# Kernel optimization log

Hardware: AMD Instinct MI355X
Metric: run time of the kernel (lower is better)

The kernel has to match this reference:

```python
import jax, jax.numpy as jnp
import numpy as np

# Complete binary Huffman tree: V leaves, V-1 internal nodes, heap-indexed
# (node 0 = root, leaf i lives at heap index V-1+i, parent(n) = (n-1)//2).
V = 32768     # vocab size (leaves)
D = 15        # path depth = log2(V) internal nodes per leaf
DM = 1024     # input word-vector dim
B = 8         # batch of input word vectors
T = 1024      # target ids per batch item


def _build_paths():
    """paths[i, l] = heap index of the l-th internal node (leaf-to-root) on leaf i's path."""
    n = np.arange(V, dtype=np.int64) + (V - 1)  # leaf heap indices
    paths = np.zeros((V, D), dtype=np.int32)
    for lvl in range(D):
        n = (n - 1) // 2
        paths[:, lvl] = n
    return jnp.asarray(paths)


def setup_inputs() -> dict:
    key = jax.random.key(0)
    k1, k2, k3 = jax.random.split(key, 3)
    x = jax.random.normal(k1, (B, DM), dtype=jnp.float32)
    ids = jax.random.randint(k2, (B, T), 0, V)
    W = jax.random.normal(k3, (V - 1, DM), dtype=jnp.float32) * 0.02  # stacked Linear(DM,1) weights
    b = jnp.zeros((V - 1,), dtype=jnp.float32)                        # stacked Linear biases
    return {"x": x, "ids": ids, "paths": _build_paths(), "W": W, "b": b}


def reference(x, ids, paths, W, b):
    # node_idx: [B, T, D] internal-node heap indices along each target's path
    node_idx = paths[ids]
    Wp = W[node_idx]                 # [B, T, D, DM] gathered per-node weight rows
    bp = b[node_idx]                 # [B, T, D]
    # per-node Linear + bias: logit = w_node . x + b_node
    logits = jnp.einsum('btdk,bk->btd', Wp, x) + bp
    # product of sigmoid branch probabilities along the path -> [B, T]
    return jnp.prod(jax.nn.sigmoid(logits), axis=-1)
```

## Files before the change

kernel.cpp:

```cpp
#include <hip/hip_runtime.h>
#include <math.h>

#define V 32768
#define D 15
#define DM 1024
#define B 8
#define T 1024
#define NNODES (V - 1)
#define R 4

typedef float vfloat4 __attribute__((ext_vector_type(4)));

__global__ __launch_bounds__(256, 4) void hsm_logits_kernel(
    const float* __restrict__ x,
    const float* __restrict__ W,
    const float* __restrict__ bias,
    float* __restrict__ sig)
{
    __shared__ vfloat4 xs[B * DM / 4];

    const vfloat4* x4 = (const vfloat4*)x;
    #pragma unroll
    for (int i = threadIdx.x; i < B * DM / 4; i += 256) xs[i] = x4[i];
    __syncthreads();

    const int wave = __builtin_amdgcn_readfirstlane(threadIdx.x >> 6);
    const int lane = threadIdx.x & 63;
    const int rowbase = blockIdx.x * 32 + wave * 8;

    const vfloat4* Wb = (const vfloat4*)W;

    vfloat4 wv[R], wvn[R];
    float acc[R * B];

    #pragma unroll
    for (int r = 0; r < R; r++) {
        int row = rowbase + r;
        if (row > NNODES - 1) row = NNODES - 1;
        wv[r] = __builtin_nontemporal_load(&Wb[(size_t)row * 256 + lane]);
    }

    auto run_pass = [&](int prow0, bool preload_next, int nrow0) {
        #pragma unroll
        for (int i = 0; i < R * B; i++) acc[i] = 0.f;
        #pragma unroll
        for (int j = 0; j < 4; j++) {
            if (j < 3) {
                #pragma unroll
                for (int r = 0; r < R; r++) {
                    int row = prow0 + r;
                    if (row > NNODES - 1) row = NNODES - 1;
                    wvn[r] = __builtin_nontemporal_load(
                        &Wb[(size_t)row * 256 + (j + 1) * 64 + lane]);
                }
            } else if (preload_next) {
                #pragma unroll
                for (int r = 0; r < R; r++) {
                    int row = nrow0 + r;
                    if (row > NNODES - 1) row = NNODES - 1;
                    wvn[r] = __builtin_nontemporal_load(
                        &Wb[(size_t)row * 256 + lane]);
                }
            }
            vfloat4 xv[B];
            #pragma unroll
            for (int b = 0; b < B; b++) xv[b] = xs[b * 256 + j * 64 + lane];
            #pragma unroll
            for (int r = 0; r < R; r++) {
                #pragma unroll
                for (int b = 0; b < B; b++) {
                    acc[r * 8 + b] += wv[r].x * xv[b].x + wv[r].y * xv[b].y +
                                      wv[r].z * xv[b].z + wv[r].w * xv[b].w;
                }
            }
            #pragma unroll
            for (int r = 0; r < R; r++) wv[r] = wvn[r];
        }
    };

#define FOLD_LEVEL(MASK, NOUT)                                   \
    _Pragma("unroll")                                            \
    for (int i = 0; i < (NOUT); i++) {                           \
        const float lo = acc[2 * i];                             \
        const float hi = acc[2 * i + 1];                         \
        const float send = (lane & (MASK)) ? lo : hi;            \
        const float keep = (lane & (MASK)) ? hi : lo;            \
        acc[i] = keep + __shfl_xor(send, (MASK), 64);            \
    }

    auto fold_store = [&](int prow0) {
        FOLD_LEVEL(1, 16)
        FOLD_LEVEL(2, 8)
        FOLD_LEVEL(4, 4)
        FOLD_LEVEL(8, 2)
        FOLD_LEVEL(16, 1)
        acc[0] += __shfl_xor(acc[0], 32, 64);
        if (lane < 32) {
            const int r = lane >> 3;
            const int b = lane & 7;
            const int row = prow0 + r;
            if (row < NNODES) {
                const float z = acc[0] + bias[row];
                sig[(size_t)row * B + b] = 1.f / (1.f + expf(-z));
            }
        }
    };

    run_pass(rowbase, true, rowbase + R);
    fold_store(rowbase);
    run_pass(rowbase + R, false, 0);
    fold_store(rowbase + R);
#undef FOLD_LEVEL
}

__global__ __launch_bounds__(256) void hsm_prod_kernel(
    const int* __restrict__ ids,
    const int* __restrict__ paths,
    const float* __restrict__ sig,
    float* __restrict__ out)
{
    const int i = blockIdx.x * blockDim.x + threadIdx.x;
    if (i >= B * T) return;
    const int b = i / T;
    const int id = ids[i];
    const int* p = paths + (size_t)id * D;
    const int4* p4 = (const int4*)p;
    int4 n0 = p4[0], n1 = p4[1], n2 = p4[2];
    float prod = 1.f;
    prod *= sig[(size_t)n0.x * B + b] * sig[(size_t)n0.y * B + b] *
            sig[(size_t)n0.z * B + b] * sig[(size_t)n0.w * B + b];
    prod *= sig[(size_t)n1.x * B + b] * sig[(size_t)n1.y * B + b] *
            sig[(size_t)n1.z * B + b] * sig[(size_t)n1.w * B + b];
    prod *= sig[(size_t)n2.x * B + b] * sig[(size_t)n2.y * B + b] *
            sig[(size_t)n2.z * B + b] * sig[(size_t)n2.w * B + b];
    prod *= sig[(size_t)p[12] * B + b] * sig[(size_t)p[13] * B + b] *
            sig[(size_t)p[14] * B + b];
    out[i] = prod;
}

extern "C" void kernel_launch(void* const* d_in, const int* in_sizes, int n_in,
                              void* d_out, int out_size, void* d_ws, size_t ws_size,
                              hipStream_t stream) {
    const float* x     = (const float*)d_in[0];
    const int*   ids   = (const int*)d_in[1];
    const int*   paths = (const int*)d_in[2];
    const float* W     = (const float*)d_in[3];
    const float* bias  = (const float*)d_in[4];
    float* out = (float*)d_out;
    float* sig = (float*)d_ws;

    const int grid1 = (V + 31) / 32;
    hsm_logits_kernel<<<grid1, 256, 0, stream>>>(x, W, bias, sig);

    const int grid2 = (B * T + 255) / 256;
    hsm_prod_kernel<<<grid2, 256, 0, stream>>>(ids, paths, sig, out);
}
```

Before: 197.6 us.

## Compute only the top tree levels densely and gather the bottom two per target

The dense logits kernel now covers only the first 8191 internal nodes (the top 13 levels) instead of all 32767. The two deepest path nodes of each target are computed on demand in the product kernel: one wave per target gathers the two weight rows and reduces the dot products with shuffles. Path nodes are derived arithmetically from the heap index rather than read from the paths table. This cuts the dense weight stream to a quarter, but adds scattered row gathers that can hit the same rows more than once, and it relies on the tree being the complete heap-indexed layout the task defines.

```diff
diff --git a/kernel.cpp b/kernel.cpp
--- a/kernel.cpp
+++ b/kernel.cpp
@@ -7,6 +7,7 @@
 #define B 8
 #define T 1024
 #define NNODES (V - 1)
+#define NK1 8191
 #define R 4
 
 typedef float vfloat4 __attribute__((ext_vector_type(4)));
@@ -36,7 +37,7 @@
     #pragma unroll
     for (int r = 0; r < R; r++) {
         int row = rowbase + r;
-        if (row > NNODES - 1) row = NNODES - 1;
+        if (row > NK1 - 1) row = NK1 - 1;
         wv[r] = __builtin_nontemporal_load(&Wb[(size_t)row * 256 + lane]);
     }
 
@@ -49,7 +50,7 @@
                 #pragma unroll
                 for (int r = 0; r < R; r++) {
                     int row = prow0 + r;
-                    if (row > NNODES - 1) row = NNODES - 1;
+                    if (row > NK1 - 1) row = NK1 - 1;
                     wvn[r] = __builtin_nontemporal_load(
                         &Wb[(size_t)row * 256 + (j + 1) * 64 + lane]);
                 }
@@ -57,7 +58,7 @@
                 #pragma unroll
                 for (int r = 0; r < R; r++) {
                     int row = nrow0 + r;
-                    if (row > NNODES - 1) row = NNODES - 1;
+                    if (row > NK1 - 1) row = NK1 - 1;
                     wvn[r] = __builtin_nontemporal_load(
                         &Wb[(size_t)row * 256 + lane]);
                 }
@@ -99,7 +100,7 @@
             const int r = lane >> 3;
             const int b = lane & 7;
             const int row = prow0 + r;
-            if (row < NNODES) {
+            if (row < NK1) {
                 const float z = acc[0] + bias[row];
                 sig[(size_t)row * B + b] = 1.f / (1.f + expf(-z));
             }
@@ -114,28 +115,61 @@
 }
 
 __global__ __launch_bounds__(256) void hsm_prod_kernel(
+    const float* __restrict__ x,
     const int* __restrict__ ids,
-    const int* __restrict__ paths,
+    const float* __restrict__ W,
+    const float* __restrict__ bias,
     const float* __restrict__ sig,
     float* __restrict__ out)
 {
-    const int i = blockIdx.x * blockDim.x + threadIdx.x;
+    const int wave = threadIdx.x >> 6;
+    const int lane = threadIdx.x & 63;
+    const int i = blockIdx.x * 4 + wave;
     if (i >= B * T) return;
-    const int b = i / T;
+    const int b = i >> 10;
     const int id = ids[i];
-    const int* p = paths + (size_t)id * D;
-    const int4* p4 = (const int4*)p;
-    int4 n0 = p4[0], n1 = p4[1], n2 = p4[2];
-    float prod = 1.f;
-    prod *= sig[(size_t)n0.x * B + b] * sig[(size_t)n0.y * B + b] *
-            sig[(size_t)n0.z * B + b] * sig[(size_t)n0.w * B + b];
-    prod *= sig[(size_t)n1.x * B + b] * sig[(size_t)n1.y * B + b] *
-            sig[(size_t)n1.z * B + b] * sig[(size_t)n1.w * B + b];
-    prod *= sig[(size_t)n2.x * B + b] * sig[(size_t)n2.y * B + b] *
-            sig[(size_t)n2.z * B + b] * sig[(size_t)n2.w * B + b];
-    prod *= sig[(size_t)p[12] * B + b] * sig[(size_t)p[13] * B + b] *
-            sig[(size_t)p[14] * B + b];
-    out[i] = prod;
+    const unsigned m = (unsigned)id + V;
+    const int r0 = (int)(m >> 1) - 1;
+    const int r1 = (int)(m >> 2) - 1;
+
+    const vfloat4* W4 = (const vfloat4*)W;
+    const vfloat4* x4 = (const vfloat4*)x;
+
+    vfloat4 w0[4], w1[4], xv[4];
+    #pragma unroll
+    for (int j = 0; j < 4; j++) w0[j] = W4[(size_t)r0 * 256 + j * 64 + lane];
+    #pragma unroll
+    for (int j = 0; j < 4; j++) w1[j] = W4[(size_t)r1 * 256 + j * 64 + lane];
+    #pragma unroll
+    for (int j = 0; j < 4; j++) xv[j] = x4[b * 256 + j * 64 + lane];
+    const float bb0 = bias[r0];
+    const float bb1 = bias[r1];
+
+    float a0 = 0.f, a1 = 0.f;
+    #pragma unroll
+    for (int j = 0; j < 4; j++) {
+        a0 += w0[j].x * xv[j].x + w0[j].y * xv[j].y + w0[j].z * xv[j].z + w0[j].w * xv[j].w;
+        a1 += w1[j].x * xv[j].x + w1[j].y * xv[j].y + w1[j].z * xv[j].z + w1[j].w * xv[j].w;
+    }
+    #pragma unroll
+    for (int s = 1; s < 64; s <<= 1) {
+        a0 += __shfl_xor(a0, s, 64);
+        a1 += __shfl_xor(a1, s, 64);
+    }
+
+    float p = 1.f;
+    if (lane < 13) {
+        const int nl = (int)(m >> (lane + 3)) - 1;
+        p = sig[(size_t)nl * B + b];
+    }
+    #pragma unroll
+    for (int s = 1; s < 16; s <<= 1) p *= __shfl_xor(p, s, 64);
+
+    if (lane == 0) {
+        const float s0 = 1.f / (1.f + expf(-(a0 + bb0)));
+        const float s1 = 1.f / (1.f + expf(-(a1 + bb1)));
+        out[i] = p * s0 * s1;
+    }
 }
 
 extern "C" void kernel_launch(void* const* d_in, const int* in_sizes, int n_in,
@@ -143,15 +177,14 @@
                               hipStream_t stream) {
     const float* x     = (const float*)d_in[0];
     const int*   ids   = (const int*)d_in[1];
-    const int*   paths = (const int*)d_in[2];
     const float* W     = (const float*)d_in[3];
     const float* bias  = (const float*)d_in[4];
     float* out = (float*)d_out;
     float* sig = (float*)d_ws;
 
-    const int grid1 = (V + 31) / 32;
+    const int grid1 = (NK1 + 31) / 32;
     hsm_logits_kernel<<<grid1, 256, 0, stream>>>(x, W, bias, sig);
 
-    const int grid2 = (B * T + 255) / 256;
-    hsm_prod_kernel<<<grid2, 256, 0, stream>>>(ids, paths, sig, out);
+    const int grid2 = (B * T) / 4;
+    hsm_prod_kernel<<<grid2, 256, 0, stream>>>(x, ids, W, bias, sig, out);
 }
```

New measurement: 195.6 us. Within noise of the previous version (-1.0%).
